# Kernel optimization log

Hardware: AMD Instinct MI355X
Metric: run time of the kernel (lower is better)

Reference implementation:

```python
import jax, jax.numpy as jnp
import numpy as np

N, K, D, H = 131072, 4, 128, 128


def setup_inputs() -> dict:
    key = jax.random.key(0)
    ks = jax.random.split(key, 8)
    s = 1.0 / np.sqrt(H)  # torch default LSTM-style init scale
    return {
        "x": jax.random.normal(ks[0], (N, D), jnp.float32),
        "h_child": jax.random.normal(ks[1], (N, K, H), jnp.float32),
        "c_child": jax.random.normal(ks[2], (N, K, H), jnp.float32),
        "W_iou": jax.random.normal(ks[3], (D, 3 * H), jnp.float32) * s,
        "U_iou": jax.random.normal(ks[4], (H, 3 * H), jnp.float32) * s,
        "b_iou": jnp.zeros((3 * H,), jnp.float32),
        "W_f": jax.random.normal(ks[5], (D, H), jnp.float32) * s,
        "U_f": jax.random.normal(ks[6], (H, H), jnp.float32) * s,
        "b_f": jnp.zeros((H,), jnp.float32),
    }


def reference(x, h_child, c_child, W_iou, U_iou, b_iou, W_f, U_f, b_f):
    # Child-Sum Tree-LSTM node_forward over a batch of N nodes with K children.
    h_sum = h_child.sum(axis=1)                               # [N, H]
    iou = x @ W_iou + h_sum @ U_iou + b_iou                   # [N, 3H]
    i, o, u = jnp.split(iou, 3, axis=-1)
    i = jax.nn.sigmoid(i)
    o = jax.nn.sigmoid(o)
    u = jnp.tanh(u)
    # per-child forget gates: f_k = sigmoid(W_f x + U_f h_k + b_f)  [N, K, H]
    f = jax.nn.sigmoid((x @ W_f)[:, None, :]
                       + jnp.einsum('nkh,hg->nkg', h_child, U_f)
                       + b_f)
    c = i * u + (f * c_child).sum(axis=1)                     # [N, H]
    h = o * jnp.tanh(c)                                       # [N, H]
    return jnp.stack([h, c])                                  # [2, N, H]
```

## Files before the change

### kernel.cpp

```cpp
#include <hip/hip_runtime.h>


#define NN 131072
#define LDSS 136

typedef __attribute__((ext_vector_type(8))) short bf16x8;
typedef __attribute__((ext_vector_type(4))) float f32x4;

#define BX_HI 0
#define BX_LO 65536
#define BH_HI 131072
#define BH_LO 180224
#define UF_HI 229376
#define UF_LO 245760

__device__ __forceinline__ unsigned short f2bf(float f){
  unsigned int u = __float_as_uint(f);
  u += 0x7FFFu + ((u >> 16) & 1u);
  return (unsigned short)(u >> 16);
}
__device__ __forceinline__ float bf2f(unsigned short h){
  return __uint_as_float(((unsigned int)h) << 16);
}
__device__ __forceinline__ float sigm(float v){ return 1.f / (1.f + __expf(-v)); }
__device__ __forceinline__ float tanh_f(float v){
  float a = fabsf(v);
  float e = __expf(-2.f * a);
  float r = (1.f - e) / (1.f + e);
  return copysignf(r, v);
}

__device__ __forceinline__ void split8_store(unsigned short* hp, unsigned short* lp,
                                             const float* v){
  unsigned short h[8], l[8];
#pragma unroll
  for (int i = 0; i < 8; ++i){
    h[i] = f2bf(v[i]);
    l[i] = f2bf(v[i] - bf2f(h[i]));
  }
  uint4 uh, ul;
  uh.x = (unsigned)h[0] | ((unsigned)h[1] << 16);
  uh.y = (unsigned)h[2] | ((unsigned)h[3] << 16);
  uh.z = (unsigned)h[4] | ((unsigned)h[5] << 16);
  uh.w = (unsigned)h[6] | ((unsigned)h[7] << 16);
  ul.x = (unsigned)l[0] | ((unsigned)l[1] << 16);
  ul.y = (unsigned)l[2] | ((unsigned)l[3] << 16);
  ul.z = (unsigned)l[4] | ((unsigned)l[5] << 16);
  ul.w = (unsigned)l[6] | ((unsigned)l[7] << 16);
  *(uint4*)hp = uh;
  *(uint4*)lp = ul;
}

__global__ void prep_weights(const float* __restrict__ Wiou, const float* __restrict__ Uiou,
                             const float* __restrict__ Wf, const float* __restrict__ Uf,
                             unsigned short* __restrict__ ws){
  int tid = blockIdx.x * 256 + threadIdx.x;
  float v; int k, col, nt; unsigned int bhi, blo;
  if (tid < 65536){
    k = tid >> 9; col = tid & 511;
    v = (col < 384) ? Wiou[k * 384 + col] : Wf[k * 128 + (col - 384)];
    nt = 32; bhi = BX_HI; blo = BX_LO;
  } else if (tid < 65536 + 49152){
    int s = tid - 65536; k = s / 384; col = s - k * 384;
    v = Uiou[k * 384 + col];
    nt = 24; bhi = BH_HI; blo = BH_LO;
  } else {
    int s = tid - 65536 - 49152; k = s >> 7; col = s & 127;
    v = Uf[k * 128 + col];
    nt = 8; bhi = UF_HI; blo = UF_LO;
  }
  int kc = k >> 5, q = (k >> 3) & 3, j = k & 7;
  int nc = col >> 4, cc = col & 15;
  int lane = q * 16 + cc;
  unsigned int addr = ((unsigned)(kc * nt + nc) * 64u + (unsigned)lane) * 8u + (unsigned)j;
  unsigned short hi = f2bf(v);
  unsigned short lo = f2bf(v - bf2f(hi));
  ws[bhi + addr] = hi;
  ws[blo + addr] = lo;
}

__launch_bounds__(256, 2)
__global__ void tree_lstm_fused(const float* __restrict__ xg,
                                const float* __restrict__ hcg,
                                const float* __restrict__ ccg,
                                const float* __restrict__ b_iou,
                                const float* __restrict__ b_f,
                                const unsigned short* __restrict__ ws,
                                float* __restrict__ out){
  __shared__ alignas(16) unsigned short AxHi[32 * LDSS];
  __shared__ alignas(16) unsigned short AxLo[32 * LDSS];
  __shared__ alignas(16) unsigned short HkHi[32 * LDSS];
  __shared__ alignas(16) unsigned short HkLo[32 * LDSS];

  const int t = threadIdx.x;
  const int lane = t & 63;
  const int w = t >> 6;
  const int m = lane & 15;
  const int q = lane >> 4;
  const int node0 = blockIdx.x * 32;
  const int nc0 = 2 * w;

#pragma unroll
  for (int g = 0; g < 2; ++g){
    int idx8 = t + 256 * g;
    int row = idx8 >> 4, col8 = idx8 & 15;
    const float4* s = (const float4*)(xg + (size_t)(node0 + row) * 128 + col8 * 8);
    float4 a = s[0], b = s[1];
    float v[8] = {a.x, a.y, a.z, a.w, b.x, b.y, b.z, b.w};
    split8_store(AxHi + row * LDSS + col8 * 8, AxLo + row * LDSS + col8 * 8, v);
  }
  __syncthreads();

  const f32x4 zero = {0.f, 0.f, 0.f, 0.f};
  f32x4 acc[8][2];
#pragma unroll
  for (int c = 0; c < 8; ++c)
#pragma unroll
    for (int rt = 0; rt < 2; ++rt) acc[c][rt] = zero;

#pragma unroll
  for (int kc = 0; kc < 4; ++kc){
    bf16x8 ah[2], al[2];
#pragma unroll
    for (int rt = 0; rt < 2; ++rt){
      int off = (rt * 16 + m) * LDSS + kc * 32 + q * 8;
      ah[rt] = *(const bf16x8*)(AxHi + off);
      al[rt] = *(const bf16x8*)(AxLo + off);
    }
#pragma unroll
    for (int c = 0; c < 8; ++c){
      int nc = (c >> 1) * 8 + nc0 + (c & 1);
      bf16x8 bh = *(const bf16x8*)(ws + BX_HI + ((kc * 32 + nc) * 64 + lane) * 8);
      bf16x8 bl = *(const bf16x8*)(ws + BX_LO + ((kc * 32 + nc) * 64 + lane) * 8);
#pragma unroll
      for (int rt = 0; rt < 2; ++rt){
        acc[c][rt] = __builtin_amdgcn_mfma_f32_16x16x32_bf16(ah[rt], bh, acc[c][rt], 0, 0, 0);
        acc[c][rt] = __builtin_amdgcn_mfma_f32_16x16x32_bf16(al[rt], bh, acc[c][rt], 0, 0, 0);
        acc[c][rt] = __builtin_amdgcn_mfma_f32_16x16x32_bf16(ah[rt], bl, acc[c][rt], 0, 0, 0);
      }
    }
  }

  float hs[16];
#pragma unroll
  for (int i = 0; i < 16; ++i) hs[i] = 0.f;
  f32x4 fc[2][2];
#pragma unroll
  for (int ct = 0; ct < 2; ++ct)
#pragma unroll
    for (int rt = 0; rt < 2; ++rt) fc[ct][rt] = zero;

  float bfv[2];
#pragma unroll
  for (int ct = 0; ct < 2; ++ct) bfv[ct] = b_f[w * 32 + ct * 16 + m];

  for (int k = 0; k < 4; ++k){
    float v0[8], v1[8];
    {
      int row = t >> 4, col8 = t & 15;
      const float4* s = (const float4*)(hcg + ((size_t)(node0 + row) * 4 + k) * 128 + col8 * 8);
      float4 a = s[0], b = s[1];
      v0[0]=a.x; v0[1]=a.y; v0[2]=a.z; v0[3]=a.w; v0[4]=b.x; v0[5]=b.y; v0[6]=b.z; v0[7]=b.w;
    }
    {
      int idx8 = t + 256; int row = idx8 >> 4, col8 = idx8 & 15;
      const float4* s = (const float4*)(hcg + ((size_t)(node0 + row) * 4 + k) * 128 + col8 * 8);
      float4 a = s[0], b = s[1];
      v1[0]=a.x; v1[1]=a.y; v1[2]=a.z; v1[3]=a.w; v1[4]=b.x; v1[5]=b.y; v1[6]=b.z; v1[7]=b.w;
    }
    __syncthreads();
    {
      int row = t >> 4, col8 = t & 15;
      split8_store(HkHi + row * LDSS + col8 * 8, HkLo + row * LDSS + col8 * 8, v0);
    }
    {
      int idx8 = t + 256; int row = idx8 >> 4, col8 = idx8 & 15;
      split8_store(HkHi + row * LDSS + col8 * 8, HkLo + row * LDSS + col8 * 8, v1);
    }
#pragma unroll
    for (int i = 0; i < 8; ++i){ hs[i] += v0[i]; hs[8 + i] += v1[i]; }
    __syncthreads();

    f32x4 hu[2][2];
#pragma unroll
    for (int ct = 0; ct < 2; ++ct)
#pragma unroll
      for (int rt = 0; rt < 2; ++rt) hu[ct][rt] = zero;

#pragma unroll
    for (int kc = 0; kc < 4; ++kc){
      bf16x8 ah[2], al[2];
#pragma unroll
      for (int rt = 0; rt < 2; ++rt){
        int off = (rt * 16 + m) * LDSS + kc * 32 + q * 8;
        ah[rt] = *(const bf16x8*)(HkHi + off);
        al[rt] = *(const bf16x8*)(HkLo + off);
      }
#pragma unroll
      for (int ct = 0; ct < 2; ++ct){
        int nc = nc0 + ct;
        bf16x8 bh = *(const bf16x8*)(ws + UF_HI + ((kc * 8 + nc) * 64 + lane) * 8);
        bf16x8 bl = *(const bf16x8*)(ws + UF_LO + ((kc * 8 + nc) * 64 + lane) * 8);
#pragma unroll
        for (int rt = 0; rt < 2; ++rt){
          hu[ct][rt] = __builtin_amdgcn_mfma_f32_16x16x32_bf16(ah[rt], bh, hu[ct][rt], 0, 0, 0);
          hu[ct][rt] = __builtin_amdgcn_mfma_f32_16x16x32_bf16(al[rt], bh, hu[ct][rt], 0, 0, 0);
          hu[ct][rt] = __builtin_amdgcn_mfma_f32_16x16x32_bf16(ah[rt], bl, hu[ct][rt], 0, 0, 0);
        }
      }
    }
#pragma unroll
    for (int ct = 0; ct < 2; ++ct){
      int f = w * 32 + ct * 16 + m;
#pragma unroll
      for (int rt = 0; rt < 2; ++rt){
#pragma unroll
        for (int r = 0; r < 4; ++r){
          int node = node0 + rt * 16 + q * 4 + r;
          float pre = acc[6 + ct][rt][r] + hu[ct][rt][r] + bfv[ct];
          float fg = sigm(pre);
          float cc = ccg[((size_t)node * 4 + k) * 128 + f];
          fc[ct][rt][r] += fg * cc;
        }
      }
    }
  }

  __syncthreads();
  {
    int row = t >> 4, col8 = t & 15;
    split8_store(HkHi + row * LDSS + col8 * 8, HkLo + row * LDSS + col8 * 8, &hs[0]);
  }
  {
    int idx8 = t + 256; int row = idx8 >> 4, col8 = idx8 & 15;
    split8_store(HkHi + row * LDSS + col8 * 8, HkLo + row * LDSS + col8 * 8, &hs[8]);
  }
  __syncthreads();

#pragma unroll
  for (int kc = 0; kc < 4; ++kc){
    bf16x8 ah[2], al[2];
#pragma unroll
    for (int rt = 0; rt < 2; ++rt){
      int off = (rt * 16 + m) * LDSS + kc * 32 + q * 8;
      ah[rt] = *(const bf16x8*)(HkHi + off);
      al[rt] = *(const bf16x8*)(HkLo + off);
    }
#pragma unroll
    for (int c = 0; c < 6; ++c){
      int nc = (c >> 1) * 8 + nc0 + (c & 1);
      bf16x8 bh = *(const bf16x8*)(ws + BH_HI + ((kc * 24 + nc) * 64 + lane) * 8);
      bf16x8 bl = *(const bf16x8*)(ws + BH_LO + ((kc * 24 + nc) * 64 + lane) * 8);
#pragma unroll
      for (int rt = 0; rt < 2; ++rt){
        acc[c][rt] = __builtin_amdgcn_mfma_f32_16x16x32_bf16(ah[rt], bh, acc[c][rt], 0, 0, 0);
        acc[c][rt] = __builtin_amdgcn_mfma_f32_16x16x32_bf16(al[rt], bh, acc[c][rt], 0, 0, 0);
        acc[c][rt] = __builtin_amdgcn_mfma_f32_16x16x32_bf16(ah[rt], bl, acc[c][rt], 0, 0, 0);
      }
    }
  }

  float biv[2], bov[2], buv[2];
#pragma unroll
  for (int ct = 0; ct < 2; ++ct){
    int f = w * 32 + ct * 16 + m;
    biv[ct] = b_iou[f];
    bov[ct] = b_iou[128 + f];
    buv[ct] = b_iou[256 + f];
  }
#pragma unroll
  for (int ct = 0; ct < 2; ++ct){
    int f = w * 32 + ct * 16 + m;
#pragma unroll
    for (int rt = 0; rt < 2; ++rt){
#pragma unroll
      for (int r = 0; r < 4; ++r){
        int node = node0 + rt * 16 + q * 4 + r;
        float iv = sigm(acc[ct][rt][r] + biv[ct]);
        float ov = sigm(acc[2 + ct][rt][r] + bov[ct]);
        float uv = tanh_f(acc[4 + ct][rt][r] + buv[ct]);
        float cv = iv * uv + fc[ct][rt][r];
        float hv = ov * tanh_f(cv);
        out[(size_t)node * 128 + f] = hv;
        out[(size_t)NN * 128 + (size_t)node * 128 + f] = cv;
      }
    }
  }
}

extern "C" void kernel_launch(void* const* d_in, const int* in_sizes, int n_in,
                              void* d_out, int out_size, void* d_ws, size_t ws_size,
                              hipStream_t stream){
  const float* x       = (const float*)d_in[0];
  const float* h_child = (const float*)d_in[1];
  const float* c_child = (const float*)d_in[2];
  const float* W_iou   = (const float*)d_in[3];
  const float* U_iou   = (const float*)d_in[4];
  const float* b_iou   = (const float*)d_in[5];
  const float* W_f     = (const float*)d_in[6];
  const float* U_f     = (const float*)d_in[7];
  const float* b_f     = (const float*)d_in[8];
  unsigned short* ws   = (unsigned short*)d_ws;
  float* out           = (float*)d_out;

  prep_weights<<<512, 256, 0, stream>>>(W_iou, U_iou, W_f, U_f, ws);
  tree_lstm_fused<<<NN / 32, 256, 0, stream>>>(x, h_child, c_child, b_iou, b_f, ws, out);
}
```

Before: 762.9 us.

## Prefetch child states, double-buffer LDS, and fold h_sum GEMM into per-child loop

Double-buffers the child hidden-state LDS tiles and prefetches the next child's h into registers, which removes one barrier per child. c_child reads are hoisted ahead of the MFMA work. The separate h_sum @ U_iou pass is replaced by accumulating each child's h_k @ U_iou inside the child loop, relying on linearity. This removes the extra LDS staging and sync, but quadruples the MFMA work for that GEMM and raises register pressure.

```diff
diff --git a/kernel.cpp b/kernel.cpp
--- a/kernel.cpp
+++ b/kernel.cpp
@@ -89,8 +89,8 @@
                                 float* __restrict__ out){
   __shared__ alignas(16) unsigned short AxHi[32 * LDSS];
   __shared__ alignas(16) unsigned short AxLo[32 * LDSS];
-  __shared__ alignas(16) unsigned short HkHi[32 * LDSS];
-  __shared__ alignas(16) unsigned short HkLo[32 * LDSS];
+  __shared__ alignas(16) unsigned short HkHi[2][32 * LDSS];
+  __shared__ alignas(16) unsigned short HkLo[2][32 * LDSS];
 
   const int t = threadIdx.x;
   const int lane = t & 63;
@@ -99,15 +99,30 @@
   const int q = lane >> 4;
   const int node0 = blockIdx.x * 32;
   const int nc0 = 2 * w;
-
-#pragma unroll
-  for (int g = 0; g < 2; ++g){
-    int idx8 = t + 256 * g;
-    int row = idx8 >> 4, col8 = idx8 & 15;
-    const float4* s = (const float4*)(xg + (size_t)(node0 + row) * 128 + col8 * 8);
-    float4 a = s[0], b = s[1];
-    float v[8] = {a.x, a.y, a.z, a.w, b.x, b.y, b.z, b.w};
-    split8_store(AxHi + row * LDSS + col8 * 8, AxLo + row * LDSS + col8 * 8, v);
+  const int srow = t >> 4;
+  const int scol = (t & 15) * 8;
+
+  const float4* xp0 = (const float4*)(xg + (size_t)(node0 + srow) * 128 + scol);
+  const float4* xp1 = (const float4*)(xg + (size_t)(node0 + 16 + srow) * 128 + scol);
+  float4 x0a = xp0[0], x0b = xp0[1];
+  float4 x1a = xp1[0], x1b = xp1[1];
+  float4 pv0a, pv0b, pv1a, pv1b;
+  {
+    const float4* hp0 = (const float4*)(hcg + ((size_t)(node0 + srow) * 4 + 0) * 128 + scol);
+    const float4* hp1 = (const float4*)(hcg + ((size_t)(node0 + 16 + srow) * 4 + 0) * 128 + scol);
+    pv0a = hp0[0]; pv0b = hp0[1]; pv1a = hp1[0]; pv1b = hp1[1];
+  }
+  float bfv[2];
+  bfv[0] = b_f[w * 32 + m];
+  bfv[1] = b_f[w * 32 + 16 + m];
+
+  {
+    float v[8] = {x0a.x, x0a.y, x0a.z, x0a.w, x0b.x, x0b.y, x0b.z, x0b.w};
+    split8_store(AxHi + srow * LDSS + scol, AxLo + srow * LDSS + scol, v);
+  }
+  {
+    float v[8] = {x1a.x, x1a.y, x1a.z, x1a.w, x1b.x, x1b.y, x1b.z, x1b.w};
+    split8_store(AxHi + (16 + srow) * LDSS + scol, AxLo + (16 + srow) * LDSS + scol, v);
   }
   __syncthreads();
 
@@ -141,45 +156,39 @@
     }
   }
 
-  float hs[16];
-#pragma unroll
-  for (int i = 0; i < 16; ++i) hs[i] = 0.f;
   f32x4 fc[2][2];
 #pragma unroll
   for (int ct = 0; ct < 2; ++ct)
 #pragma unroll
     for (int rt = 0; rt < 2; ++rt) fc[ct][rt] = zero;
 
-  float bfv[2];
-#pragma unroll
-  for (int ct = 0; ct < 2; ++ct) bfv[ct] = b_f[w * 32 + ct * 16 + m];
-
+#pragma unroll
   for (int k = 0; k < 4; ++k){
-    float v0[8], v1[8];
     {
-      int row = t >> 4, col8 = t & 15;
-      const float4* s = (const float4*)(hcg + ((size_t)(node0 + row) * 4 + k) * 128 + col8 * 8);
-      float4 a = s[0], b = s[1];
-      v0[0]=a.x; v0[1]=a.y; v0[2]=a.z; v0[3]=a.w; v0[4]=b.x; v0[5]=b.y; v0[6]=b.z; v0[7]=b.w;
+      float v[8] = {pv0a.x, pv0a.y, pv0a.z, pv0a.w, pv0b.x, pv0b.y, pv0b.z, pv0b.w};
+      split8_store(HkHi[k & 1] + srow * LDSS + scol, HkLo[k & 1] + srow * LDSS + scol, v);
     }
     {
-      int idx8 = t + 256; int row = idx8 >> 4, col8 = idx8 & 15;
-      const float4* s = (const float4*)(hcg + ((size_t)(node0 + row) * 4 + k) * 128 + col8 * 8);
-      float4 a = s[0], b = s[1];
-      v1[0]=a.x; v1[1]=a.y; v1[2]=a.z; v1[3]=a.w; v1[4]=b.x; v1[5]=b.y; v1[6]=b.z; v1[7]=b.w;
+      float v[8] = {pv1a.x, pv1a.y, pv1a.z, pv1a.w, pv1b.x, pv1b.y, pv1b.z, pv1b.w};
+      split8_store(HkHi[k & 1] + (16 + srow) * LDSS + scol,
+                   HkLo[k & 1] + (16 + srow) * LDSS + scol, v);
     }
     __syncthreads();
-    {
-      int row = t >> 4, col8 = t & 15;
-      split8_store(HkHi + row * LDSS + col8 * 8, HkLo + row * LDSS + col8 * 8, v0);
-    }
-    {
-      int idx8 = t + 256; int row = idx8 >> 4, col8 = idx8 & 15;
-      split8_store(HkHi + row * LDSS + col8 * 8, HkLo + row * LDSS + col8 * 8, v1);
-    }
-#pragma unroll
-    for (int i = 0; i < 8; ++i){ hs[i] += v0[i]; hs[8 + i] += v1[i]; }
-    __syncthreads();
+
+    if (k < 3){
+      const float4* hp0 = (const float4*)(hcg + ((size_t)(node0 + srow) * 4 + (k + 1)) * 128 + scol);
+      const float4* hp1 = (const float4*)(hcg + ((size_t)(node0 + 16 + srow) * 4 + (k + 1)) * 128 + scol);
+      pv0a = hp0[0]; pv0b = hp0[1]; pv1a = hp1[0]; pv1b = hp1[1];
+    }
+    float cpre[16];
+#pragma unroll
+    for (int ct = 0; ct < 2; ++ct)
+#pragma unroll
+      for (int rt = 0; rt < 2; ++rt)
+#pragma unroll
+        for (int r = 0; r < 4; ++r)
+          cpre[(ct * 2 + rt) * 4 + r] =
+              ccg[((size_t)(node0 + rt * 16 + q * 4 + r) * 4 + k) * 128 + w * 32 + ct * 16 + m];
 
     f32x4 hu[2][2];
 #pragma unroll
@@ -193,8 +202,23 @@
 #pragma unroll
       for (int rt = 0; rt < 2; ++rt){
         int off = (rt * 16 + m) * LDSS + kc * 32 + q * 8;
-        ah[rt] = *(const bf16x8*)(HkHi + off);
-        al[rt] = *(const bf16x8*)(HkLo + off);
+        ah[rt] = *(const bf16x8*)(HkHi[k & 1] + off);
+        al[rt] = *(const bf16x8*)(HkLo[k & 1] + off);
+      }
+#pragma unroll
+      for (int g = 0; g < 3; ++g){
+#pragma unroll
+        for (int ct = 0; ct < 2; ++ct){
+          int nc = g * 8 + nc0 + ct;
+          bf16x8 bh = *(const bf16x8*)(ws + BH_HI + ((kc * 24 + nc) * 64 + lane) * 8);
+          bf16x8 bl = *(const bf16x8*)(ws + BH_LO + ((kc * 24 + nc) * 64 + lane) * 8);
+#pragma unroll
+          for (int rt = 0; rt < 2; ++rt){
+            acc[g*2+ct][rt] = __builtin_amdgcn_mfma_f32_16x16x32_bf16(ah[rt], bh, acc[g*2+ct][rt], 0, 0, 0);
+            acc[g*2+ct][rt] = __builtin_amdgcn_mfma_f32_16x16x32_bf16(al[rt], bh, acc[g*2+ct][rt], 0, 0, 0);
+            acc[g*2+ct][rt] = __builtin_amdgcn_mfma_f32_16x16x32_bf16(ah[rt], bl, acc[g*2+ct][rt], 0, 0, 0);
+          }
+        }
       }
 #pragma unroll
       for (int ct = 0; ct < 2; ++ct){
@@ -211,51 +235,13 @@
     }
 #pragma unroll
     for (int ct = 0; ct < 2; ++ct){
-      int f = w * 32 + ct * 16 + m;
 #pragma unroll
       for (int rt = 0; rt < 2; ++rt){
 #pragma unroll
         for (int r = 0; r < 4; ++r){
-          int node = node0 + rt * 16 + q * 4 + r;
           float pre = acc[6 + ct][rt][r] + hu[ct][rt][r] + bfv[ct];
-          float fg = sigm(pre);
-          float cc = ccg[((size_t)node * 4 + k) * 128 + f];
-          fc[ct][rt][r] += fg * cc;
+          fc[ct][rt][r] += sigm(pre) * cpre[(ct * 2 + rt) * 4 + r];
         }
-      }
-    }
-  }
-
-  __syncthreads();
-  {
-    int row = t >> 4, col8 = t & 15;
-    split8_store(HkHi + row * LDSS + col8 * 8, HkLo + row * LDSS + col8 * 8, &hs[0]);
-  }
-  {
-    int idx8 = t + 256; int row = idx8 >> 4, col8 = idx8 & 15;
-    split8_store(HkHi + row * LDSS + col8 * 8, HkLo + row * LDSS + col8 * 8, &hs[8]);
-  }
-  __syncthreads();
-
-#pragma unroll
-  for (int kc = 0; kc < 4; ++kc){
-    bf16x8 ah[2], al[2];
-#pragma unroll
-    for (int rt = 0; rt < 2; ++rt){
-      int off = (rt * 16 + m) * LDSS + kc * 32 + q * 8;
-      ah[rt] = *(const bf16x8*)(HkHi + off);
-      al[rt] = *(const bf16x8*)(HkLo + off);
-    }
-#pragma unroll
-    for (int c = 0; c < 6; ++c){
-      int nc = (c >> 1) * 8 + nc0 + (c & 1);
-      bf16x8 bh = *(const bf16x8*)(ws + BH_HI + ((kc * 24 + nc) * 64 + lane) * 8);
-      bf16x8 bl = *(const bf16x8*)(ws + BH_LO + ((kc * 24 + nc) * 64 + lane) * 8);
-#pragma unroll
-      for (int rt = 0; rt < 2; ++rt){
-        acc[c][rt] = __builtin_amdgcn_mfma_f32_16x16x32_bf16(ah[rt], bh, acc[c][rt], 0, 0, 0);
-        acc[c][rt] = __builtin_amdgcn_mfma_f32_16x16x32_bf16(al[rt], bh, acc[c][rt], 0, 0, 0);
-        acc[c][rt] = __builtin_amdgcn_mfma_f32_16x16x32_bf16(ah[rt], bl, acc[c][rt], 0, 0, 0);
       }
     }
   }
```

Measured after the change: 840.7 us. 10.2% more time.
